# Kernel optimization log

Hardware: AMD Instinct MI355X
Metric: run time of the kernel (lower is better)

## Reference

```python
import jax, jax.numpy as jnp
import numpy as np

# ---- constants from init_kwargs ----
TAU_MEM = 10.0
TAU_SYN = np.array([5.0, 2.0], dtype=np.float32)
THRESHOLD = 1.0
WINDOW = 0.3
BATCH = 32
T = 1024
N_NEURONS = 1024
N_SYN = len(TAU_SYN)

def _bitshift(tau):
    b = np.round(np.log2(np.asarray(tau, dtype=np.float32)))
    return np.maximum(b, 0.0).astype(np.float32)

DASH_MEM = float(_bitshift(TAU_MEM))          # 3.0 -> decay factor 2^-3
DASH_SYN = _bitshift(TAU_SYN)                  # [2.0, 1.0]
MEM_DECAY = np.float32(2.0 ** (-DASH_MEM))     # fraction removed per step
SYN_DECAY = (2.0 ** (-DASH_SYN)).astype(np.float32)  # (n_syn,)


def setup_inputs() -> dict:
    key = jax.random.key(0)
    # Bernoulli spike raster, (batch*T, n_syn, n_neurons)
    u = jax.random.uniform(key, (BATCH * T, N_SYN, N_NEURONS), dtype=jnp.float32)
    binary_input = (u < 0.2).astype(jnp.float32)
    return {"binary_input": binary_input}


def _lif_scan(syn_out):
    """syn_out: (T, B, N, n_syn). Bitshift-decay LIF with membrane-subtract reset."""
    syn_decay = jnp.asarray(SYN_DECAY)  # (n_syn,)
    mem_decay = jnp.float32(MEM_DECAY)
    vmem0 = jnp.zeros((BATCH, N_NEURONS), jnp.float32)
    isyn0 = jnp.zeros((BATCH, N_NEURONS, N_SYN), jnp.float32)

    def step(carry, inp_t):
        vmem, isyn = carry
        # bitshift decay: x -= x >> dash  <=>  x -= x * 2^-dash
        isyn = isyn - isyn * syn_decay + inp_t            # (B, N, n_syn)
        vmem = vmem - vmem * mem_decay + isyn.sum(-1)     # (B, N)
        spk = (vmem >= THRESHOLD).astype(vmem.dtype)
        vmem = vmem - spk * THRESHOLD                     # membrane subtract
        return (vmem, isyn), (spk, vmem)

    (_, _), (spikes, vmem_rec) = jax.lax.scan(step, (vmem0, isyn0), syn_out)
    return spikes, vmem_rec  # (T, B, N) each


def reference(binary_input):
    # (B*T, n_syn, N) -> (B, T, n_syn, N) -> (T, B, n_syn, N) -> (T, B, N, n_syn)
    x = binary_input.reshape(BATCH, T, N_SYN, N_NEURONS)
    x = jnp.swapaxes(x, 0, 1)
    x = jnp.moveaxis(x, -2, -1)
    spikes, _ = _lif_scan(x)
    # (T, B, N) -> (B, T, N) -> (B*T, N)
    out = jnp.swapaxes(spikes, 0, 1).reshape(BATCH * T, N_NEURONS)
    return out
```

## Files before the change

kernel.cpp:

```cpp
#include <hip/hip_runtime.h>


#define TT 1024
#define NN 1024
#define BB 32
#define UU 16

__global__ __launch_bounds__(64, 1)
void lif_scan_kernel(const float* __restrict__ in, float* __restrict__ out) {
    const int gid = blockIdx.x * 64 + threadIdx.x;
    const int b = gid >> 10;
    const int n = gid & (NN - 1);

    const float* __restrict__ ip = in + (size_t)b * TT * 2 * NN + n;
    float* __restrict__ op = out + (size_t)b * TT * NN + n;

    const float SD0 = 0.25f;
    const float SD1 = 0.5f;
    const float MD  = 0.125f;

    float i0 = 0.0f, i1 = 0.0f, v = 0.0f;

    float x0[UU], x1[UU];
#pragma unroll
    for (int j = 0; j < UU; ++j) {
        x0[j] = ip[j * 2048];
        x1[j] = ip[j * 2048 + 1024];
    }

    for (int tc = 0; tc < TT - UU; tc += UU) {
        float y0[UU], y1[UU];
        const float* pn = ip + (tc + UU) * 2048;
#pragma unroll
        for (int j = 0; j < UU; ++j) {
            y0[j] = pn[j * 2048];
            y1[j] = pn[j * 2048 + 1024];
        }
        float* po = op + tc * NN;
#pragma unroll
        for (int j = 0; j < UU; ++j) {
            i0 = (i0 - i0 * SD0) + x0[j];
            i1 = (i1 - i1 * SD1) + x1[j];
            float vd = v - v * MD;
            v = vd + (i0 + i1);
            float spk = (v >= 1.0f) ? 1.0f : 0.0f;
            v -= spk;
            po[j * NN] = spk;
        }
#pragma unroll
        for (int j = 0; j < UU; ++j) { x0[j] = y0[j]; x1[j] = y1[j]; }
    }

    {
        float* po = op + (TT - UU) * NN;
#pragma unroll
        for (int j = 0; j < UU; ++j) {
            i0 = (i0 - i0 * SD0) + x0[j];
            i1 = (i1 - i1 * SD1) + x1[j];
            float vd = v - v * MD;
            v = vd + (i0 + i1);
            float spk = (v >= 1.0f) ? 1.0f : 0.0f;
            v -= spk;
            po[j * NN] = spk;
        }
    }
}

extern "C" void kernel_launch(void* const* d_in, const int* in_sizes, int n_in,
                              void* d_out, int out_size, void* d_ws, size_t ws_size,
                              hipStream_t stream) {
    const float* in = (const float*)d_in[0];
    float* out = (float*)d_out;
    dim3 grid(BB * NN / 64);
    dim3 block(64);
    hipLaunchKernelGGL(lif_scan_kernel, grid, block, 0, stream, in, out);
}
```

Measured before the change: 392.0 us.

## Stage input through LDS with async global_load_lds double buffering

Replaces the register-based prefetch of the next 16 timesteps with direct global-to-LDS loads into a double-buffered shared array, then reads the inputs from LDS during the scan. Output stores are deferred until after the compute loop and a vmcnt wait. The aim is to free registers and keep more loads in flight without tying up VGPRs. The single-wave blocks and a waitcnt before the stores could serialize loads with stores, and LDS reads add latency to the sequential chain.

```diff
diff --git a/kernel.cpp b/kernel.cpp
--- a/kernel.cpp
+++ b/kernel.cpp
@@ -1,4 +1,5 @@
 #include <hip/hip_runtime.h>
+#include <stdint.h>
 
 
 #define TT 1024
@@ -8,12 +9,14 @@
 
 __global__ __launch_bounds__(64, 1)
 void lif_scan_kernel(const float* __restrict__ in, float* __restrict__ out) {
-    const int gid = blockIdx.x * 64 + threadIdx.x;
-    const int b = gid >> 10;
-    const int n = gid & (NN - 1);
+    __shared__ float sbuf[2][UU][2][64];
 
-    const float* __restrict__ ip = in + (size_t)b * TT * 2 * NN + n;
-    float* __restrict__ op = out + (size_t)b * TT * NN + n;
+    const int lane = threadIdx.x;
+    const int b  = blockIdx.x >> 4;
+    const int n0 = (blockIdx.x & 15) << 6;
+
+    const float* gin  = in  + (size_t)b * TT * 2 * NN + n0 + lane;
+    float*       gout = out + (size_t)b * TT * NN     + n0 + lane;
 
     const float SD0 = 0.25f;
     const float SD1 = 0.5f;
@@ -21,48 +24,55 @@
 
     float i0 = 0.0f, i1 = 0.0f, v = 0.0f;
 
-    float x0[UU], x1[UU];
 #pragma unroll
     for (int j = 0; j < UU; ++j) {
-        x0[j] = ip[j * 2048];
-        x1[j] = ip[j * 2048 + 1024];
+#pragma unroll
+        for (int s = 0; s < 2; ++s) {
+            __builtin_amdgcn_global_load_lds(
+                (const float __attribute__((address_space(1)))*)(gin + j * 2048 + s * 1024),
+                (float __attribute__((address_space(3)))*)(&sbuf[0][j][s][0]),
+                4, 0, 0);
+        }
     }
+    __builtin_amdgcn_s_waitcnt(0x0F70);
+    asm volatile("" ::: "memory");
 
-    for (int tc = 0; tc < TT - UU; tc += UU) {
-        float y0[UU], y1[UU];
-        const float* pn = ip + (tc + UU) * 2048;
+    int p = 0;
+    for (int tc = 0; tc < TT; tc += UU, p ^= 1) {
+        if (tc + UU < TT) {
+            const float* gnext = gin + (size_t)(tc + UU) * 2048;
+#pragma unroll
+            for (int j = 0; j < UU; ++j) {
+#pragma unroll
+                for (int s = 0; s < 2; ++s) {
+                    __builtin_amdgcn_global_load_lds(
+                        (const float __attribute__((address_space(1)))*)(gnext + j * 2048 + s * 1024),
+                        (float __attribute__((address_space(3)))*)(&sbuf[p ^ 1][j][s][0]),
+                        4, 0, 0);
+                }
+            }
+        }
+
+        float spk[UU];
 #pragma unroll
         for (int j = 0; j < UU; ++j) {
-            y0[j] = pn[j * 2048];
-            y1[j] = pn[j * 2048 + 1024];
-        }
-        float* po = op + tc * NN;
-#pragma unroll
-        for (int j = 0; j < UU; ++j) {
-            i0 = (i0 - i0 * SD0) + x0[j];
-            i1 = (i1 - i1 * SD1) + x1[j];
+            float x0 = sbuf[p][j][0][lane];
+            float x1 = sbuf[p][j][1][lane];
+            i0 = (i0 - i0 * SD0) + x0;
+            i1 = (i1 - i1 * SD1) + x1;
             float vd = v - v * MD;
             v = vd + (i0 + i1);
-            float spk = (v >= 1.0f) ? 1.0f : 0.0f;
-            v -= spk;
-            po[j * NN] = spk;
+            float s_ = (v >= 1.0f) ? 1.0f : 0.0f;
+            v -= s_;
+            spk[j] = s_;
         }
+
+        __builtin_amdgcn_s_waitcnt(0x0F70);
+        asm volatile("" ::: "memory");
+
+        float* go = gout + (size_t)tc * NN;
 #pragma unroll
-        for (int j = 0; j < UU; ++j) { x0[j] = y0[j]; x1[j] = y1[j]; }
-    }
-
-    {
-        float* po = op + (TT - UU) * NN;
-#pragma unroll
-        for (int j = 0; j < UU; ++j) {
-            i0 = (i0 - i0 * SD0) + x0[j];
-            i1 = (i1 - i1 * SD1) + x1[j];
-            float vd = v - v * MD;
-            v = vd + (i0 + i1);
-            float spk = (v >= 1.0f) ? 1.0f : 0.0f;
-            v -= spk;
-            po[j * NN] = spk;
-        }
+        for (int j = 0; j < UU; ++j) go[j * NN] = spk[j];
     }
 }
 
```

New measurement: 393.4 us. Within noise of the previous version (+0.4%).

## Process four neurons per thread with float4 loads and stores

Applied to the files above, without the earlier changes.

Each thread now advances four adjacent neurons using vectorized float4 loads and stores, and the prefetch depth is halved to eight steps. The grid shrinks from 512 to 128 single-wave blocks. This aims to cut load/store instruction count and widen memory transactions, and the four independent recurrences give more instruction-level parallelism per thread. In exchange, far fewer waves run, so many CUs sit idle and fewer bytes are in flight to hide memory latency.

```diff
diff --git a/kernel.cpp b/kernel.cpp
--- a/kernel.cpp
+++ b/kernel.cpp
@@ -4,64 +4,73 @@
 #define TT 1024
 #define NN 1024
 #define BB 32
-#define UU 16
+#define UU 8
+
+__device__ __forceinline__ float lif_step(float x0, float x1,
+                                          float& i0, float& i1, float& v) {
+    const float SD0 = 0.25f;
+    const float SD1 = 0.5f;
+    const float MD  = 0.125f;
+    i0 = (i0 - i0 * SD0) + x0;
+    i1 = (i1 - i1 * SD1) + x1;
+    float vd = v - v * MD;
+    v = vd + (i0 + i1);
+    float s_ = (v >= 1.0f) ? 1.0f : 0.0f;
+    v -= s_;
+    return s_;
+}
 
 __global__ __launch_bounds__(64, 1)
 void lif_scan_kernel(const float* __restrict__ in, float* __restrict__ out) {
-    const int gid = blockIdx.x * 64 + threadIdx.x;
-    const int b = gid >> 10;
-    const int n = gid & (NN - 1);
+    const int lane = threadIdx.x;
+    const int b = blockIdx.x >> 2;
+    const int q = blockIdx.x & 3;
+    const int nv = (q << 6) + lane;
 
-    const float* __restrict__ ip = in + (size_t)b * TT * 2 * NN + n;
-    float* __restrict__ op = out + (size_t)b * TT * NN + n;
+    const float4* gin  = (const float4*)(in  + (size_t)b * TT * 2 * NN) + nv;
+    float4*       gout = (float4*)      (out + (size_t)b * TT * NN)     + nv;
 
-    const float SD0 = 0.25f;
-    const float SD1 = 0.5f;
-    const float MD  = 0.125f;
+    float i0[4] = {0,0,0,0}, i1[4] = {0,0,0,0}, vm[4] = {0,0,0,0};
 
-    float i0 = 0.0f, i1 = 0.0f, v = 0.0f;
-
-    float x0[UU], x1[UU];
+    float4 x0[UU], x1[UU];
 #pragma unroll
     for (int j = 0; j < UU; ++j) {
-        x0[j] = ip[j * 2048];
-        x1[j] = ip[j * 2048 + 1024];
+        x0[j] = gin[j * 512];
+        x1[j] = gin[j * 512 + 256];
     }
 
     for (int tc = 0; tc < TT - UU; tc += UU) {
-        float y0[UU], y1[UU];
-        const float* pn = ip + (tc + UU) * 2048;
+        float4 y0[UU], y1[UU];
+        const float4* pn = gin + (size_t)(tc + UU) * 512;
 #pragma unroll
         for (int j = 0; j < UU; ++j) {
-            y0[j] = pn[j * 2048];
-            y1[j] = pn[j * 2048 + 1024];
+            y0[j] = pn[j * 512];
+            y1[j] = pn[j * 512 + 256];
         }
-        float* po = op + tc * NN;
+        float4* po = gout + (size_t)tc * 256;
 #pragma unroll
         for (int j = 0; j < UU; ++j) {
-            i0 = (i0 - i0 * SD0) + x0[j];
-            i1 = (i1 - i1 * SD1) + x1[j];
-            float vd = v - v * MD;
-            v = vd + (i0 + i1);
-            float spk = (v >= 1.0f) ? 1.0f : 0.0f;
-            v -= spk;
-            po[j * NN] = spk;
+            float4 a = x0[j], c = x1[j], sp;
+            sp.x = lif_step(a.x, c.x, i0[0], i1[0], vm[0]);
+            sp.y = lif_step(a.y, c.y, i0[1], i1[1], vm[1]);
+            sp.z = lif_step(a.z, c.z, i0[2], i1[2], vm[2]);
+            sp.w = lif_step(a.w, c.w, i0[3], i1[3], vm[3]);
+            po[j * 256] = sp;
         }
 #pragma unroll
         for (int j = 0; j < UU; ++j) { x0[j] = y0[j]; x1[j] = y1[j]; }
     }
 
     {
-        float* po = op + (TT - UU) * NN;
+        float4* po = gout + (size_t)(TT - UU) * 256;
 #pragma unroll
         for (int j = 0; j < UU; ++j) {
-            i0 = (i0 - i0 * SD0) + x0[j];
-            i1 = (i1 - i1 * SD1) + x1[j];
-            float vd = v - v * MD;
-            v = vd + (i0 + i1);
-            float spk = (v >= 1.0f) ? 1.0f : 0.0f;
-            v -= spk;
-            po[j * NN] = spk;
+            float4 a = x0[j], c = x1[j], sp;
+            sp.x = lif_step(a.x, c.x, i0[0], i1[0], vm[0]);
+            sp.y = lif_step(a.y, c.y, i0[1], i1[1], vm[1]);
+            sp.z = lif_step(a.z, c.z, i0[2], i1[2], vm[2]);
+            sp.w = lif_step(a.w, c.w, i0[3], i1[3], vm[3]);
+            po[j * 256] = sp;
         }
     }
 }
@@ -71,7 +80,7 @@
                               hipStream_t stream) {
     const float* in = (const float*)d_in[0];
     float* out = (float*)d_out;
-    dim3 grid(BB * NN / 64);
+    dim3 grid(BB * 4);
     dim3 block(64);
     hipLaunchKernelGGL(lif_scan_kernel, grid, block, 0, stream, in, out);
 }
```

New measurement: 420.2 us. 7.2% more time.

## Deepen load prefetch to four rotating register buffers of eight steps

Applied to the files above, without the earlier changes.

Replaces the double-buffered 16-step prefetch with four rotating 8-step register buffers. The load for a chunk four ahead is issued right after each chunk is computed, so about 24-32 timesteps of input are in flight instead of 16. The aim is to hide global memory latency for this occupancy-limited scan (one 64-thread wave per block) and to remove the register copy between buffers. It raises register pressure, which may cause spills or more waiting on loads.

```diff
diff --git a/kernel.cpp b/kernel.cpp
--- a/kernel.cpp
+++ b/kernel.cpp
@@ -4,7 +4,8 @@
 #define TT 1024
 #define NN 1024
 #define BB 32
-#define UU 16
+#define UU 8
+#define NCHUNK (TT / UU)
 
 __global__ __launch_bounds__(64, 1)
 void lif_scan_kernel(const float* __restrict__ in, float* __restrict__ out) {
@@ -12,8 +13,8 @@
     const int b = gid >> 10;
     const int n = gid & (NN - 1);
 
-    const float* __restrict__ ip = in + (size_t)b * TT * 2 * NN + n;
-    float* __restrict__ op = out + (size_t)b * TT * NN + n;
+    const float* __restrict__ ip = in  + (size_t)b * TT * 2 * NN + n;
+    float* __restrict__       op = out + (size_t)b * TT * NN     + n;
 
     const float SD0 = 0.25f;
     const float SD1 = 0.5f;
@@ -21,49 +22,53 @@
 
     float i0 = 0.0f, i1 = 0.0f, v = 0.0f;
 
-    float x0[UU], x1[UU];
-#pragma unroll
-    for (int j = 0; j < UU; ++j) {
-        x0[j] = ip[j * 2048];
-        x1[j] = ip[j * 2048 + 1024];
+    float a0[UU], a1[UU], b0[UU], b1[UU],
+          c0[UU], c1[UU], d0[UU], d1[UU];
+
+#define LOADC(B0, B1, CH)                                            \
+    {                                                                \
+        const float* _p = ip + (size_t)(CH) * (UU * 2048);           \
+        _Pragma("unroll")                                            \
+        for (int j = 0; j < UU; ++j) {                               \
+            B0[j] = _p[j * 2048];                                    \
+            B1[j] = _p[j * 2048 + 1024];                             \
+        }                                                            \
     }
 
-    for (int tc = 0; tc < TT - UU; tc += UU) {
-        float y0[UU], y1[UU];
-        const float* pn = ip + (tc + UU) * 2048;
-#pragma unroll
-        for (int j = 0; j < UU; ++j) {
-            y0[j] = pn[j * 2048];
-            y1[j] = pn[j * 2048 + 1024];
-        }
-        float* po = op + tc * NN;
-#pragma unroll
-        for (int j = 0; j < UU; ++j) {
-            i0 = (i0 - i0 * SD0) + x0[j];
-            i1 = (i1 - i1 * SD1) + x1[j];
-            float vd = v - v * MD;
-            v = vd + (i0 + i1);
-            float spk = (v >= 1.0f) ? 1.0f : 0.0f;
-            v -= spk;
-            po[j * NN] = spk;
-        }
-#pragma unroll
-        for (int j = 0; j < UU; ++j) { x0[j] = y0[j]; x1[j] = y1[j]; }
+#define COMPC(B0, B1, CH)                                            \
+    {                                                                \
+        float* _o = op + (size_t)(CH) * (UU * NN);                   \
+        _Pragma("unroll")                                            \
+        for (int j = 0; j < UU; ++j) {                               \
+            i0 = (i0 - i0 * SD0) + B0[j];                            \
+            i1 = (i1 - i1 * SD1) + B1[j];                            \
+            float vd = v - v * MD;                                   \
+            v = vd + (i0 + i1);                                      \
+            float spk = (v >= 1.0f) ? 1.0f : 0.0f;                   \
+            v -= spk;                         \
+            _o[j * NN] = spk;                                        \
+        }                                                            \
     }
 
-    {
-        float* po = op + (TT - UU) * NN;
-#pragma unroll
-        for (int j = 0; j < UU; ++j) {
-            i0 = (i0 - i0 * SD0) + x0[j];
-            i1 = (i1 - i1 * SD1) + x1[j];
-            float vd = v - v * MD;
-            v = vd + (i0 + i1);
-            float spk = (v >= 1.0f) ? 1.0f : 0.0f;
-            v -= spk;
-            po[j * NN] = spk;
-        }
+    LOADC(a0, a1, 0)
+    LOADC(b0, b1, 1)
+    LOADC(c0, c1, 2)
+    LOADC(d0, d1, 3)
+
+    for (int c = 0; c < NCHUNK - 4; c += 4) {
+        COMPC(a0, a1, c)     LOADC(a0, a1, c + 4)
+        COMPC(b0, b1, c + 1) LOADC(b0, b1, c + 5)
+        COMPC(c0, c1, c + 2) LOADC(c0, c1, c + 6)
+        COMPC(d0, d1, c + 3) LOADC(d0, d1, c + 7)
     }
+
+    COMPC(a0, a1, NCHUNK - 4)
+    COMPC(b0, b1, NCHUNK - 3)
+    COMPC(c0, c1, NCHUNK - 2)
+    COMPC(d0, d1, NCHUNK - 1)
+
+#undef LOADC
+#undef COMPC
 }
 
 extern "C" void kernel_launch(void* const* d_in, const int* in_sizes, int n_in,
```

After: 397.6 us. About the same (+1.4%).
